# Kernel optimization log

Hardware: AMD Instinct MI355X
Metric: run time of the kernel (lower is better)

The kernel has to match this reference:

```python
import jax, jax.numpy as jnp
import numpy as np

BATCH = 16384
IN_DIM = 256
UNITS = 256


def setup_inputs() -> dict:
    key = jax.random.key(0)
    ks = jax.random.split(key, 5)
    scale = 1.0 / np.sqrt(IN_DIM + UNITS)
    return {
        "x": jax.random.normal(ks[0], (BATCH, IN_DIM), dtype=jnp.float32),
        "prev_h": jax.random.normal(ks[1], (BATCH, UNITS), dtype=jnp.float32),
        "Wz": jax.random.normal(ks[2], (IN_DIM + UNITS, UNITS), dtype=jnp.float32) * scale,
        "bz": jnp.zeros((UNITS,), dtype=jnp.float32),
        "Wr": jax.random.normal(ks[3], (IN_DIM + UNITS, UNITS), dtype=jnp.float32) * scale,
        "br": jnp.zeros((UNITS,), dtype=jnp.float32),
        "Ws": jax.random.normal(ks[4], (IN_DIM + UNITS, UNITS), dtype=jnp.float32) * scale,
        "bs": jnp.zeros((UNITS,), dtype=jnp.float32),
    }


def reference(x, prev_h, Wz, bz, Wr, br, Ws, bs):
    # concat order matches the TF module: [prev_h, x]
    concat = jnp.concatenate([prev_h, x], axis=1)  # [B, units+in_dim]
    z = jax.nn.sigmoid(concat @ Wz + bz)
    r = jax.nn.sigmoid(concat @ Wr + br)
    concat_cand = jnp.concatenate([r * prev_h, x], axis=1)
    h_tilda = jnp.tanh(concat_cand @ Ws + bs)
    h_new = (1.0 - z) * prev_h + z * h_tilda
    return h_new
```

## Files before the change

### kernel.cpp

```cpp
#include <hip/hip_runtime.h>
#include <hip/hip_bf16.h>


#define BATCH 16384
#define UNITS 256
#define KDIM 512
#define ROWS 64

typedef float f32x4 __attribute__((ext_vector_type(4)));
typedef __bf16 bf16x8 __attribute__((ext_vector_type(8)));
typedef unsigned short us8 __attribute__((ext_vector_type(8)));
typedef unsigned short us4v __attribute__((ext_vector_type(4)));

static __device__ __forceinline__ unsigned short f2bf(float f) {
    union { float f; unsigned u; } v; v.f = f;
    unsigned r = v.u + 0x7fffu + ((v.u >> 16) & 1u);
    return (unsigned short)(r >> 16);
}
static __device__ __forceinline__ float bf2f(unsigned short u) {
    union { unsigned u; float f; } v; v.u = ((unsigned)u) << 16;
    return v.f;
}

__global__ void pack_weights(const float* __restrict__ Wz,
                             const float* __restrict__ Wr,
                             const float* __restrict__ Ws,
                             unsigned short* __restrict__ out) {
    int gid = blockIdx.x * blockDim.x + threadIdx.x;
    int w   = gid >> 17;
    int rem = gid & 131071;
    int k = rem >> 8;
    int n = rem & 255;
    const float* W = (w == 0) ? Wz : (w == 1) ? Wr : Ws;
    float f = W[rem];
    int kt = k >> 5, kr = k & 31;
    int hi = kr >> 3, j = kr & 7;
    int nt = n >> 4,  lo = n & 15;
    int l  = hi * 16 + lo;
    out[(size_t)w * 131072 + (size_t)(((kt * 16 + nt) * 64 + l) * 8 + j)] = f2bf(f);
}

__launch_bounds__(1024, 4)
__global__ void gru_main(const float* __restrict__ x,
                         const float* __restrict__ ph,
                         const float* __restrict__ bz,
                         const float* __restrict__ br,
                         const float* __restrict__ bs,
                         const unsigned short* __restrict__ Wp,
                         float* __restrict__ out) {
    __shared__ unsigned short sm[ROWS * 512];
    __shared__ unsigned short rh[ROWS * 256];

    const int tid  = threadIdx.x;
    const int lane = tid & 63;
    const int wid  = tid >> 6;
    const int brow = blockIdx.x * ROWS;

    const int l15 = lane & 15;
    const int kg  = (lane >> 4) << 3;
    const int col = wid * 16 + l15;

    const unsigned short* Wz_p = Wp;
    const unsigned short* Wr_p = Wp + 131072;
    const unsigned short* Ws_p = Wp + 262144;
    const unsigned short* pz = Wz_p + (size_t)((wid * 64 + lane) * 8);
    const unsigned short* pr = Wr_p + (size_t)((wid * 64 + lane) * 8);
    const unsigned short* ps = Ws_p + (size_t)((wid * 64 + lane) * 8);
    us8 b0n = *(const us8*)pz;
    us8 b1n = *(const us8*)pr;
    float bzc = bz[col], brc = br[col], bsc = bs[col];

    for (int i = tid; i < 4096; i += 1024) {
        int row = i >> 6;
        int c4  = (i & 63) << 2;
        int swr = (row & 7) << 3;
        float4 a = *(const float4*)&ph[(size_t)(brow + row) * 256 + c4];
        us4v u; u.x = f2bf(a.x); u.y = f2bf(a.y); u.z = f2bf(a.z); u.w = f2bf(a.w);
        *(us4v*)&sm[row * 512 + (c4 ^ swr)] = u;
        float4 b = *(const float4*)&x[(size_t)(brow + row) * 256 + c4];
        us4v v; v.x = f2bf(b.x); v.y = f2bf(b.y); v.z = f2bf(b.z); v.w = f2bf(b.w);
        *(us4v*)&sm[row * 512 + ((256 + c4) ^ swr)] = v;
    }
    __syncthreads();

    f32x4 accz[4] = {};
    f32x4 accr[4] = {};
#pragma unroll 4
    for (int kt = 0; kt < 16; ++kt) {
        bf16x8 B0 = __builtin_bit_cast(bf16x8, b0n);
        bf16x8 B1 = __builtin_bit_cast(bf16x8, b1n);
        if (kt < 15) {
            b0n = *(const us8*)(pz + (size_t)(kt + 1) * 8192);
            b1n = *(const us8*)(pr + (size_t)(kt + 1) * 8192);
        }
        int ak = kt * 32 + kg;
#pragma unroll
        for (int m = 0; m < 4; ++m) {
            int arow = m * 16 + l15;
            bf16x8 a = __builtin_bit_cast(bf16x8,
                *(const us8*)&sm[arow * 512 + (ak ^ ((arow & 7) << 3))]);
            accz[m] = __builtin_amdgcn_mfma_f32_16x16x32_bf16(a, B0, accz[m], 0, 0, 0);
            accr[m] = __builtin_amdgcn_mfma_f32_16x16x32_bf16(a, B1, accr[m], 0, 0, 0);
        }
    }

    us8 s0n = *(const us8*)ps;
    us8 s1n = *(const us8*)(ps + 8192);

    float pst[4][4];
    const int rrow0 = (lane >> 4) * 4;
#pragma unroll
    for (int m = 0; m < 4; ++m) {
#pragma unroll
        for (int i = 0; i < 4; ++i) {
            int lrow = m * 16 + rrow0 + i;
            int cs = col ^ ((lrow & 7) << 3);
            float p = bf2f(sm[lrow * 512 + cs]);
            float z = 1.f / (1.f + __expf(-(accz[m][i] + bzc)));
            float r = 1.f / (1.f + __expf(-(accr[m][i] + brc)));
            accz[m][i] = z;
            pst[m][i]  = p;
            rh[lrow * 256 + cs] = f2bf(r * p);
        }
    }
    __syncthreads();

    f32x4 accs[4] = {};
#pragma unroll 4
    for (int kt = 0; kt < 8; ++kt) {
        bf16x8 B = __builtin_bit_cast(bf16x8, s0n);
        s0n = s1n;
        s1n = *(const us8*)(ps + (size_t)(kt + 2) * 8192);
        int ak = kt * 32 + kg;
#pragma unroll
        for (int m = 0; m < 4; ++m) {
            int arow = m * 16 + l15;
            bf16x8 a = __builtin_bit_cast(bf16x8,
                *(const us8*)&rh[arow * 256 + (ak ^ ((arow & 7) << 3))]);
            accs[m] = __builtin_amdgcn_mfma_f32_16x16x32_bf16(a, B, accs[m], 0, 0, 0);
        }
    }
#pragma unroll 4
    for (int kt = 8; kt < 16; ++kt) {
        bf16x8 B = __builtin_bit_cast(bf16x8, s0n);
        s0n = s1n;
        if (kt < 14) s1n = *(const us8*)(ps + (size_t)(kt + 2) * 8192);
        int ak = kt * 32 + kg;
#pragma unroll
        for (int m = 0; m < 4; ++m) {
            int arow = m * 16 + l15;
            bf16x8 a = __builtin_bit_cast(bf16x8,
                *(const us8*)&sm[arow * 512 + (ak ^ ((arow & 7) << 3))]);
            accs[m] = __builtin_amdgcn_mfma_f32_16x16x32_bf16(a, B, accs[m], 0, 0, 0);
        }
    }

#pragma unroll
    for (int m = 0; m < 4; ++m) {
#pragma unroll
        for (int i = 0; i < 4; ++i) {
            float s = accs[m][i] + bsc;
            float e = __expf(-2.f * fabsf(s));
            float th = (1.f - e) / (1.f + e);
            th = (s < 0.f) ? -th : th;
            float z = accz[m][i];
            float p = pst[m][i];
            int grow = brow + m * 16 + rrow0 + i;
            out[(size_t)grow * 256 + col] = (1.f - z) * p + z * th;
        }
    }
}

extern "C" void kernel_launch(void* const* d_in, const int* in_sizes, int n_in,
                              void* d_out, int out_size, void* d_ws, size_t ws_size,
                              hipStream_t stream) {
    const float* x  = (const float*)d_in[0];
    const float* ph = (const float*)d_in[1];
    const float* Wz = (const float*)d_in[2];
    const float* bz = (const float*)d_in[3];
    const float* Wr = (const float*)d_in[4];
    const float* br = (const float*)d_in[5];
    const float* Ws = (const float*)d_in[6];
    const float* bs = (const float*)d_in[7];
    unsigned short* Wp = (unsigned short*)d_ws;

    hipLaunchKernelGGL(pack_weights, dim3(1536), dim3(256), 0, stream, Wz, Wr, Ws, Wp);
    hipLaunchKernelGGL(gru_main, dim3(256), dim3(1024), 0, stream,
                       x, ph, bz, br, bs, Wp, (float*)d_out);
}
```

Baseline: 34.11 us.

## Overlap x staging with prev_h GEMM half and vectorize weight packing

The main kernel now stages only prev_h into shared memory first, issues the x loads into registers, and runs the prev_h half of the z/r GEMM before converting and storing x, so global load latency is hidden behind MFMA work. The x-part of the candidate GEMM is moved ahead of the barrier that publishes r*h, letting it overlap with the gate epilogue. The weight pack kernel now has each thread gather 8 k-values and emit one 16-byte store, using 8x fewer threads. f2bf now uses the compiler's __bf16 conversion in place of manual rounding. The cost is more live registers for the x prefetch and an extra barrier, under a 1024-thread block.

```diff
diff --git a/kernel.cpp b/kernel.cpp
--- a/kernel.cpp
+++ b/kernel.cpp
@@ -2,9 +2,6 @@
 #include <hip/hip_bf16.h>
 
 
-#define BATCH 16384
-#define UNITS 256
-#define KDIM 512
 #define ROWS 64
 
 typedef float f32x4 __attribute__((ext_vector_type(4)));
@@ -13,9 +10,8 @@
 typedef unsigned short us4v __attribute__((ext_vector_type(4)));
 
 static __device__ __forceinline__ unsigned short f2bf(float f) {
-    union { float f; unsigned u; } v; v.f = f;
-    unsigned r = v.u + 0x7fffu + ((v.u >> 16) & 1u);
-    return (unsigned short)(r >> 16);
+    __bf16 h = (__bf16)f;
+    return __builtin_bit_cast(unsigned short, h);
 }
 static __device__ __forceinline__ float bf2f(unsigned short u) {
     union { unsigned u; float f; } v; v.u = ((unsigned)u) << 16;
@@ -27,17 +23,19 @@
                              const float* __restrict__ Ws,
                              unsigned short* __restrict__ out) {
     int gid = blockIdx.x * blockDim.x + threadIdx.x;
-    int w   = gid >> 17;
-    int rem = gid & 131071;
-    int k = rem >> 8;
-    int n = rem & 255;
+    int w    = gid >> 14;
+    int rem  = gid & 16383;
+    int kt   = rem >> 10;
+    int rem2 = rem & 1023;
+    int nt   = rem2 >> 6;
+    int lane = rem2 & 63;
+    int hi = lane >> 4, lo = lane & 15;
     const float* W = (w == 0) ? Wz : (w == 1) ? Wr : Ws;
-    float f = W[rem];
-    int kt = k >> 5, kr = k & 31;
-    int hi = kr >> 3, j = kr & 7;
-    int nt = n >> 4,  lo = n & 15;
-    int l  = hi * 16 + lo;
-    out[(size_t)w * 131072 + (size_t)(((kt * 16 + nt) * 64 + l) * 8 + j)] = f2bf(f);
+    const float* src = W + (size_t)(kt * 32 + hi * 8) * 256 + nt * 16 + lo;
+    us8 o;
+#pragma unroll
+    for (int j = 0; j < 8; ++j) o[j] = f2bf(src[(size_t)j * 256]);
+    *(us8*)&out[(size_t)w * 131072 + (size_t)(((kt * 16 + nt) * 64 + lane) * 8)] = o;
 }
 
 __launch_bounds__(1024, 4)
@@ -60,33 +58,70 @@
     const int kg  = (lane >> 4) << 3;
     const int col = wid * 16 + l15;
 
-    const unsigned short* Wz_p = Wp;
-    const unsigned short* Wr_p = Wp + 131072;
-    const unsigned short* Ws_p = Wp + 262144;
-    const unsigned short* pz = Wz_p + (size_t)((wid * 64 + lane) * 8);
-    const unsigned short* pr = Wr_p + (size_t)((wid * 64 + lane) * 8);
-    const unsigned short* ps = Ws_p + (size_t)((wid * 64 + lane) * 8);
+    const unsigned short* pz = Wp          + (size_t)((wid * 64 + lane) * 8);
+    const unsigned short* pr = Wp + 131072 + (size_t)((wid * 64 + lane) * 8);
+    const unsigned short* ps = Wp + 262144 + (size_t)((wid * 64 + lane) * 8);
     us8 b0n = *(const us8*)pz;
     us8 b1n = *(const us8*)pr;
     float bzc = bz[col], brc = br[col], bsc = bs[col];
 
-    for (int i = tid; i < 4096; i += 1024) {
+#pragma unroll
+    for (int it = 0; it < 4; ++it) {
+        int i   = tid + it * 1024;
         int row = i >> 6;
         int c4  = (i & 63) << 2;
         int swr = (row & 7) << 3;
         float4 a = *(const float4*)&ph[(size_t)(brow + row) * 256 + c4];
         us4v u; u.x = f2bf(a.x); u.y = f2bf(a.y); u.z = f2bf(a.z); u.w = f2bf(a.w);
         *(us4v*)&sm[row * 512 + (c4 ^ swr)] = u;
-        float4 b = *(const float4*)&x[(size_t)(brow + row) * 256 + c4];
-        us4v v; v.x = f2bf(b.x); v.y = f2bf(b.y); v.z = f2bf(b.z); v.w = f2bf(b.w);
-        *(us4v*)&sm[row * 512 + ((256 + c4) ^ swr)] = v;
     }
     __syncthreads();
+
+    float4 xr[4];
+#pragma unroll
+    for (int it = 0; it < 4; ++it) {
+        int i   = tid + it * 1024;
+        int row = i >> 6;
+        int c4  = (i & 63) << 2;
+        xr[it] = *(const float4*)&x[(size_t)(brow + row) * 256 + c4];
+    }
 
     f32x4 accz[4] = {};
     f32x4 accr[4] = {};
 #pragma unroll 4
-    for (int kt = 0; kt < 16; ++kt) {
+    for (int kt = 0; kt < 8; ++kt) {
+        bf16x8 B0 = __builtin_bit_cast(bf16x8, b0n);
+        bf16x8 B1 = __builtin_bit_cast(bf16x8, b1n);
+        b0n = *(const us8*)(pz + (size_t)(kt + 1) * 8192);
+        b1n = *(const us8*)(pr + (size_t)(kt + 1) * 8192);
+        int ak = kt * 32 + kg;
+#pragma unroll
+        for (int m = 0; m < 4; ++m) {
+            int arow = m * 16 + l15;
+            bf16x8 a = __builtin_bit_cast(bf16x8,
+                *(const us8*)&sm[arow * 512 + (ak ^ ((arow & 7) << 3))]);
+            accz[m] = __builtin_amdgcn_mfma_f32_16x16x32_bf16(a, B0, accz[m], 0, 0, 0);
+            accr[m] = __builtin_amdgcn_mfma_f32_16x16x32_bf16(a, B1, accr[m], 0, 0, 0);
+        }
+    }
+
+#pragma unroll
+    for (int it = 0; it < 4; ++it) {
+        int i   = tid + it * 1024;
+        int row = i >> 6;
+        int c4  = (i & 63) << 2;
+        int swr = (row & 7) << 3;
+        us4v v; v.x = f2bf(xr[it].x); v.y = f2bf(xr[it].y);
+        v.z = f2bf(xr[it].z); v.w = f2bf(xr[it].w);
+        *(us4v*)&sm[row * 512 + ((256 + c4) ^ swr)] = v;
+    }
+    __syncthreads();
+
+    us8 s0n = *(const us8*)(ps + (size_t)8 * 8192);
+    us8 s1n = *(const us8*)(ps + (size_t)9 * 8192);
+
+#pragma unroll 4
+    for (int kt = 8; kt < 16; ++kt) {
         bf16x8 B0 = __builtin_bit_cast(bf16x8, b0n);
         bf16x8 B1 = __builtin_bit_cast(bf16x8, b1n);
         if (kt < 15) {
@@ -103,9 +138,6 @@
             accr[m] = __builtin_amdgcn_mfma_f32_16x16x32_bf16(a, B1, accr[m], 0, 0, 0);
         }
     }
-
-    us8 s0n = *(const us8*)ps;
-    us8 s1n = *(const us8*)(ps + 8192);
 
     float pst[4][4];
     const int rrow0 = (lane >> 4) * 4;
@@ -123,34 +155,35 @@
             rh[lrow * 256 + cs] = f2bf(r * p);
         }
     }
+
+    f32x4 accs[4] = {};
+#pragma unroll 4
+    for (int kt = 8; kt < 16; ++kt) {
+        bf16x8 B = __builtin_bit_cast(bf16x8, s0n);
+        s0n = s1n;
+        s1n = *(const us8*)(ps + (size_t)((kt + 2) & 15) * 8192);
+        int ak = kt * 32 + kg;
+#pragma unroll
+        for (int m = 0; m < 4; ++m) {
+            int arow = m * 16 + l15;
+            bf16x8 a = __builtin_bit_cast(bf16x8,
+                *(const us8*)&sm[arow * 512 + (ak ^ ((arow & 7) << 3))]);
+            accs[m] = __builtin_amdgcn_mfma_f32_16x16x32_bf16(a, B, accs[m], 0, 0, 0);
+        }
+    }
     __syncthreads();
 
-    f32x4 accs[4] = {};
 #pragma unroll 4
     for (int kt = 0; kt < 8; ++kt) {
         bf16x8 B = __builtin_bit_cast(bf16x8, s0n);
         s0n = s1n;
-        s1n = *(const us8*)(ps + (size_t)(kt + 2) * 8192);
+        if (kt < 6) s1n = *(const us8*)(ps + (size_t)(kt + 2) * 8192);
         int ak = kt * 32 + kg;
 #pragma unroll
         for (int m = 0; m < 4; ++m) {
             int arow = m * 16 + l15;
             bf16x8 a = __builtin_bit_cast(bf16x8,
                 *(const us8*)&rh[arow * 256 + (ak ^ ((arow & 7) << 3))]);
-            accs[m] = __builtin_amdgcn_mfma_f32_16x16x32_bf16(a, B, accs[m], 0, 0, 0);
-        }
-    }
-#pragma unroll 4
-    for (int kt = 8; kt < 16; ++kt) {
-        bf16x8 B = __builtin_bit_cast(bf16x8, s0n);
-        s0n = s1n;
-        if (kt < 14) s1n = *(const us8*)(ps + (size_t)(kt + 2) * 8192);
-        int ak = kt * 32 + kg;
-#pragma unroll
-        for (int m = 0; m < 4; ++m) {
-            int arow = m * 16 + l15;
-            bf16x8 a = __builtin_bit_cast(bf16x8,
-                *(const us8*)&sm[arow * 512 + (ak ^ ((arow & 7) << 3))]);
             accs[m] = __builtin_amdgcn_mfma_f32_16x16x32_bf16(a, B, accs[m], 0, 0, 0);
         }
     }
@@ -184,7 +217,7 @@
     const float* bs = (const float*)d_in[7];
     unsigned short* Wp = (unsigned short*)d_ws;
 
-    hipLaunchKernelGGL(pack_weights, dim3(1536), dim3(256), 0, stream, Wz, Wr, Ws, Wp);
+    hipLaunchKernelGGL(pack_weights, dim3(192), dim3(256), 0, stream, Wz, Wr, Ws, Wp);
     hipLaunchKernelGGL(gru_main, dim3(256), dim3(1024), 0, stream,
                        x, ph, bz, br, bs, Wp, (float*)d_out);
 }
```

Measured after the change: 33.62 us. Within noise of the previous version (-1.4%).
